# Kernel tuning notes

Hardware: AMD Instinct MI355X
Metric: run time of the kernel (lower is better)

Reference implementation:

```python
import jax, jax.numpy as jnp
import numpy as np

N_EMBD = 1024
N_HEADS = 16
HEAD_SIZE = N_EMBD // N_HEADS
BLOCK_SIZE = 2048
BATCH = 2
SEQ = 2048
EPS = 1e-5


def setup_inputs() -> dict:
    key = jax.random.key(0)
    ks = jax.random.split(key, 12)
    s = 0.02
    x = jax.random.normal(ks[0], (BATCH, SEQ, N_EMBD), dtype=jnp.float32)
    # per-head Q/K/V weights concatenated: [n_embd, n_heads*head_size]
    Wq = jax.random.normal(ks[1], (N_EMBD, N_EMBD), dtype=jnp.float32) * s
    Wk = jax.random.normal(ks[2], (N_EMBD, N_EMBD), dtype=jnp.float32) * s
    Wv = jax.random.normal(ks[3], (N_EMBD, N_EMBD), dtype=jnp.float32) * s
    Wproj = jax.random.normal(ks[4], (N_EMBD, N_EMBD), dtype=jnp.float32) * s
    bproj = jnp.zeros((N_EMBD,), dtype=jnp.float32)
    W1 = jax.random.normal(ks[5], (N_EMBD, 4 * N_EMBD), dtype=jnp.float32) * s
    b1 = jnp.zeros((4 * N_EMBD,), dtype=jnp.float32)
    W2 = jax.random.normal(ks[6], (4 * N_EMBD, N_EMBD), dtype=jnp.float32) * s
    b2 = jnp.zeros((N_EMBD,), dtype=jnp.float32)
    ln1_w = jnp.ones((N_EMBD,), dtype=jnp.float32)
    ln1_b = jnp.zeros((N_EMBD,), dtype=jnp.float32)
    ln2_w = jnp.ones((N_EMBD,), dtype=jnp.float32)
    ln2_b = jnp.zeros((N_EMBD,), dtype=jnp.float32)
    return dict(x=x, Wq=Wq, Wk=Wk, Wv=Wv, Wproj=Wproj, bproj=bproj,
                W1=W1, b1=b1, W2=W2, b2=b2,
                ln1_w=ln1_w, ln1_b=ln1_b, ln2_w=ln2_w, ln2_b=ln2_b)


def _layer_norm(x, w, b):
    mu = jnp.mean(x, axis=-1, keepdims=True)
    var = jnp.var(x, axis=-1, keepdims=True)
    return (x - mu) * jax.lax.rsqrt(var + EPS) * w + b


def reference(x, Wq, Wk, Wv, Wproj, bproj, W1, b1, W2, b2, ln1_w, ln1_b, ln2_w, ln2_b):
    B, T, C = x.shape
    # --- attention sub-block (pre-LN) ---
    h = _layer_norm(x, ln1_w, ln1_b)
    # project then split heads: [B,T,H,D] -> [B,H,T,D]
    def split(W):
        return (h @ W).reshape(B, T, N_HEADS, HEAD_SIZE).transpose(0, 2, 1, 3)
    q, k, v = split(Wq), split(Wk), split(Wv)
    # NOTE: original code scales by C**-0.5 with C = n_embd (not head_size)
    scores = jnp.einsum('bhtd,bhsd->bhts', q, k) * (C ** -0.5)  # [B,H,T,T]
    causal = jnp.tril(jnp.ones((T, T), dtype=bool))
    scores = jnp.where(causal, scores, -jnp.inf)
    wei = jax.nn.softmax(scores, axis=-1)
    attn = jnp.einsum('bhts,bhsd->bhtd', wei, v)  # [B,H,T,D]
    attn = attn.transpose(0, 2, 1, 3).reshape(B, T, C)  # concat heads
    x = x + attn @ Wproj + bproj
    # --- FFN sub-block (pre-LN) ---
    h2 = _layer_norm(x, ln2_w, ln2_b)
    ff = jax.nn.relu(h2 @ W1 + b1) @ W2 + b2
    return x + ff
```

## Files before the change

### kernel.cpp

```cpp
#include <hip/hip_runtime.h>
#include <cstdint>

typedef __attribute__((ext_vector_type(8))) __bf16 bf16_8;
typedef __attribute__((ext_vector_type(4))) __bf16 bf16_4;
typedef __attribute__((ext_vector_type(4))) float f32x4;

#define QSCALE 0.045084220027780106f

__device__ __forceinline__ void gld_lds16(const __bf16* g, __bf16* l) {
  __builtin_amdgcn_global_load_lds(
      (const __attribute__((address_space(1))) void*)(void*)g,
      (__attribute__((address_space(3))) void*)l, 16, 0, 0);
}

__global__ __launch_bounds__(256) void convt_k(
    const float* __restrict__ Wq, const float* __restrict__ Wk,
    const float* __restrict__ Wv, const float* __restrict__ Wp,
    const float* __restrict__ W1, const float* __restrict__ W2,
    __bf16* __restrict__ WqT, __bf16* __restrict__ WkT,
    __bf16* __restrict__ WvT, __bf16* __restrict__ WpT,
    __bf16* __restrict__ W1T, __bf16* __restrict__ W2T) {
  int bid = blockIdx.x;
  const float* in; __bf16* outp; int Kd, Nd, tile;
  if (bid < 4096) {
    int m = bid >> 10; tile = bid & 1023; Kd = 1024; Nd = 1024;
    in   = m == 0 ? Wq  : m == 1 ? Wk  : m == 2 ? Wv  : Wp;
    outp = m == 0 ? WqT : m == 1 ? WkT : m == 2 ? WvT : WpT;
  } else if (bid < 8192) {
    tile = bid - 4096; Kd = 1024; Nd = 4096; in = W1; outp = W1T;
  } else {
    tile = bid - 8192; Kd = 4096; Nd = 1024; in = W2; outp = W2T;
  }
  int tilesN = Nd >> 5;
  int tk = tile / tilesN, tn = tile % tilesN;
  int k0 = tk * 32, n0 = tn * 32;
  __shared__ float tbuf[32][33];
  int tx = threadIdx.x & 31, ty = threadIdx.x >> 5;
#pragma unroll
  for (int i = 0; i < 4; ++i)
    tbuf[ty + i * 8][tx] = in[(size_t)(k0 + ty + i * 8) * Nd + (n0 + tx)];
  __syncthreads();
#pragma unroll
  for (int i = 0; i < 4; ++i)
    outp[(size_t)(n0 + ty + i * 8) * Kd + (k0 + tx)] = (__bf16)tbuf[tx][ty + i * 8];
}

__global__ __launch_bounds__(256) void ln_k(const float* __restrict__ x,
                                            const float* __restrict__ w,
                                            const float* __restrict__ b,
                                            __bf16* __restrict__ out) {
  int row = blockIdx.x;
  int tid = threadIdx.x;
  f32x4 v = *(const f32x4*)(x + (size_t)row * 1024 + tid * 4);
  float s = v[0] + v[1] + v[2] + v[3];
  float sq = v[0] * v[0] + v[1] * v[1] + v[2] * v[2] + v[3] * v[3];
#pragma unroll
  for (int m = 1; m < 64; m <<= 1) { s += __shfl_xor(s, m); sq += __shfl_xor(sq, m); }
  __shared__ float rs[4], rq[4];
  int wave = tid >> 6, lane = tid & 63;
  if (lane == 0) { rs[wave] = s; rq[wave] = sq; }
  __syncthreads();
  s  = rs[0] + rs[1] + rs[2] + rs[3];
  sq = rq[0] + rq[1] + rq[2] + rq[3];
  float mu   = s * (1.f / 1024.f);
  float var  = sq * (1.f / 1024.f) - mu * mu;
  float rstd = rsqrtf(var + 1e-5f);
  f32x4 wv = *(const f32x4*)(w + tid * 4);
  f32x4 bv = *(const f32x4*)(b + tid * 4);
  bf16_4 o;
#pragma unroll
  for (int i = 0; i < 4; ++i) o[i] = (__bf16)((v[i] - mu) * rstd * wv[i] + bv[i]);
  *(bf16_4*)(out + (size_t)row * 1024 + tid * 4) = o;
}

template <int MODE, int BM, int BN, int BK>
__global__ __launch_bounds__(256) void gemm_k(
    const __bf16* __restrict__ A,
    const __bf16* __restrict__ B0, const __bf16* __restrict__ B1,
    const __bf16* __restrict__ B2,
    __bf16* __restrict__ O0, __bf16* __restrict__ O1, __bf16* __restrict__ O2,
    float* __restrict__ Of,
    const float* __restrict__ bias, const float* __restrict__ res,
    int K, int Nchunk, int nBlkM, int nBlkN) {
  constexpr int NC = BK / 8;
  constexpr int MT = BM / 32, NT = BN / 32;
  constexpr int KK = BK / 32;
  constexpr int RPC = 64 / NC;
  constexpr int CA = BM / RPC / 4;
  constexpr int CB = BN / RPC / 4;
  __shared__ __align__(16) __bf16 As[2][BM * BK];
  __shared__ __align__(16) __bf16 Bs[2][BN * BK];
  int chunk = blockIdx.y;
  const __bf16* Bt = chunk == 0 ? B0 : (chunk == 1 ? B1 : B2);
  __bf16* Ob       = chunk == 0 ? O0 : (chunk == 1 ? O1 : O2);
  int pid = blockIdx.x;
  const int GM = 8;
  int perG = GM * nBlkN;
  int gid = pid / perG;
  int fm = gid * GM;
  int gsz = min(nBlkM - fm, GM);
  int bm = fm + (pid % gsz);
  int bn = (pid % perG) / gsz;
  int m0 = bm * BM, n0 = bn * BN;
  int tid = threadIdx.x, wave = tid >> 6, lane = tid & 63;
  int quad = lane >> 4, l16 = lane & 15;
  int wm = (wave & 1) * (BM / 2), wn = (wave >> 1) * (BN / 2);
  int srow = lane / NC, schunk = lane % NC;

  f32x4 z = {0.f, 0.f, 0.f, 0.f};
  f32x4 acc[MT][NT];
#pragma unroll
  for (int mt = 0; mt < MT; ++mt)
#pragma unroll
    for (int nt = 0; nt < NT; ++nt) acc[mt][nt] = z;

  const __bf16* Ag = A  + (size_t)m0 * K;
  const __bf16* Bg = Bt + (size_t)n0 * K;

  auto stage = [&](int k0, int buf) {
#pragma unroll
    for (int i = 0; i < CA; ++i) {
      int r0 = (wave * CA + i) * RPC;
      int gc = schunk ^ ((r0 + srow) & (NC - 1));
      gld_lds16(Ag + (size_t)(r0 + srow) * K + k0 + gc * 8, &As[buf][r0 * BK]);
    }
#pragma unroll
    for (int i = 0; i < CB; ++i) {
      int r0 = (wave * CB + i) * RPC;
      int gc = schunk ^ ((r0 + srow) & (NC - 1));
      gld_lds16(Bg + (size_t)(r0 + srow) * K + k0 + gc * 8, &Bs[buf][r0 * BK]);
    }
  };

  auto compute = [&](int buf) {
#pragma unroll
    for (int kk = 0; kk < KK; ++kk) {
      bf16_8 af[MT], bfr[NT];
#pragma unroll
      for (int t = 0; t < MT; ++t) {
        int r = wm + t * 16 + l16;
        int lc = (kk * 4 + quad) ^ (r & (NC - 1));
        af[t] = *(const bf16_8*)(&As[buf][r * BK + lc * 8]);
      }
#pragma unroll
      for (int t = 0; t < NT; ++t) {
        int r = wn + t * 16 + l16;
        int lc = (kk * 4 + quad) ^ (r & (NC - 1));
        bfr[t] = *(const bf16_8*)(&Bs[buf][r * BK + lc * 8]);
      }
#pragma unroll
      for (int mt = 0; mt < MT; ++mt)
#pragma unroll
        for (int nt = 0; nt < NT; ++nt)
          acc[mt][nt] = __builtin_amdgcn_mfma_f32_16x16x32_bf16(af[mt], bfr[nt],
                                                                acc[mt][nt], 0, 0, 0);
    }
  };

  int niter = K / BK;
  stage(0, 0);
  __syncthreads();
  for (int it = 0; it < niter - 1; ++it) {
    stage((it + 1) * BK, (it + 1) & 1);
    compute(it & 1);
    __syncthreads();
  }
  compute((niter - 1) & 1);

  if (MODE == 0 && chunk == 2) {
#pragma unroll
    for (int mt = 0; mt < MT; ++mt) {
      int mbase = m0 + wm + mt * 16 + quad * 4;
      int bb = mbase >> 11, tt = mbase & 2047;
#pragma unroll
      for (int nt = 0; nt < NT; ++nt) {
        int n = n0 + wn + nt * 16 + l16;
        bf16_4 pk;
#pragma unroll
        for (int r = 0; r < 4; ++r) pk[r] = (__bf16)acc[mt][nt][r];
        *(bf16_4*)(O2 + ((size_t)((bb * 16 + (n >> 6)) * 64 + (n & 63))) * 2048 + tt) = pk;
      }
    }
    return;
  }

  float oscale = (MODE == 0 && chunk == 0) ? QSCALE : 1.0f;
#pragma unroll
  for (int mt = 0; mt < MT; ++mt) {
#pragma unroll
    for (int r = 0; r < 4; ++r) {
      int m = m0 + wm + mt * 16 + quad * 4 + r;
      size_t rowo = (size_t)m * Nchunk;
#pragma unroll
      for (int nt = 0; nt < NT; ++nt) {
        int n = n0 + wn + nt * 16 + l16;
        float v = acc[mt][nt][r];
        if (MODE == 0) {
          Ob[rowo + n] = (__bf16)(v * oscale);
        } else if (MODE == 1) {
          v += bias[n]; v = v > 0.f ? v : 0.f;
          Ob[rowo + n] = (__bf16)v;
        } else {
          v += bias[n] + res[rowo + n];
          Of[rowo + n] = v;
        }
      }
    }
  }
}

__global__ __launch_bounds__(256) void attn_k(const __bf16* __restrict__ Q,
                                              const __bf16* __restrict__ K,
                                              const __bf16* __restrict__ Vt,
                                              __bf16* __restrict__ O) {
  __shared__ __align__(16) __bf16 Kls[2][64 * 64];
  __shared__ __align__(16) __bf16 Vls[2][64 * 64];
  __shared__ __align__(16) __bf16 Pls[4][16 * 72];

  int blk = blockIdx.x;
  int qt = blk & 31, bh = blk >> 5;
  int h = bh & 15, b = bh >> 4;
  int q0 = qt * 64;
  int tid = threadIdx.x, wave = tid >> 6, lane = tid & 63;
  int quad = lane >> 4, l16 = lane & 15;
  int qw = q0 + wave * 16;
  int qrow = qw + l16;
  int r8 = lane >> 3, c8 = lane & 7;
  int cswz = c8 ^ r8;
  int so0 = (quad ^ (l16 & 7)) * 8;
  int so1 = so0 ^ 32;

  const __bf16* Qg = Q + ((size_t)(b * 2048 + qw + l16)) * 1024 + h * 64;
  bf16_8 qf0 = *(const bf16_8*)(Qg + quad * 8);
  bf16_8 qf1 = *(const bf16_8*)(Qg + 32 + quad * 8);

  const __bf16* Kb = K + (size_t)(b * 2048) * 1024 + h * 64;
  const __bf16* Vh = Vt + (size_t)((b * 16 + h) * 64) * 2048;

  f32x4 z = {0.f, 0.f, 0.f, 0.f};
  f32x4 ot[4];
#pragma unroll
  for (int dt = 0; dt < 4; ++dt) ot[dt] = z;
  float l_acc = 0.f;
  __bf16* Pw = &Pls[wave][0];

  auto stage = [&](int kt, int buf) {
#pragma unroll
    for (int i = 0; i < 2; ++i) {
      int rl = wave * 16 + i * 8 + r8;
      gld_lds16(Kb + (size_t)(kt + rl) * 1024 + cswz * 8,
                &Kls[buf][(wave * 16 + i * 8) * 64]);
      gld_lds16(Vh + (size_t)rl * 2048 + kt + cswz * 8,
                &Vls[buf][(wave * 16 + i * 8) * 64]);
    }
  };

  auto body = [&](int kt, int buf, bool masked) {
    f32x4 sf[4];
#pragma unroll
    for (int kk = 0; kk < 4; ++kk) {
      const __bf16* kr = &Kls[buf][(kk * 16 + l16) * 64];
      bf16_8 ka = *(const bf16_8*)(kr + so0);
      bf16_8 kb = *(const bf16_8*)(kr + so1);
      f32x4 a = z;
      a = __builtin_amdgcn_mfma_f32_16x16x32_bf16(ka, qf0, a, 0, 0, 0);
      a = __builtin_amdgcn_mfma_f32_16x16x32_bf16(kb, qf1, a, 0, 0, 0);
      sf[kk] = a;
    }
#pragma unroll
    for (int kk = 0; kk < 4; ++kk) {
      bf16_4 pk;
#pragma unroll
      for (int r = 0; r < 4; ++r) {
        float x = sf[kk][r];
        if (masked && (kt + kk * 16 + quad * 4 + r > qrow)) x = -1e30f;
        float p = __builtin_amdgcn_exp2f(x);
        l_acc += p;
        pk[r] = (__bf16)p;
      }
      *(bf16_4*)(Pw + l16 * 72 + kk * 16 + quad * 4) = pk;
    }
    bf16_8 pf0 = *(const bf16_8*)(Pw + l16 * 72 + quad * 8);
    bf16_8 pf1 = *(const bf16_8*)(Pw + l16 * 72 + 32 + quad * 8);
#pragma unroll
    for (int dt = 0; dt < 4; ++dt) {
      const __bf16* vr = &Vls[buf][(dt * 16 + l16) * 64];
      bf16_8 v0 = *(const bf16_8*)(vr + so0);
      bf16_8 v1 = *(const bf16_8*)(vr + so1);
      ot[dt] = __builtin_amdgcn_mfma_f32_16x16x32_bf16(v0, pf0, ot[dt], 0, 0, 0);
      ot[dt] = __builtin_amdgcn_mfma_f32_16x16x32_bf16(v1, pf1, ot[dt], 0, 0, 0);
    }
  };

  stage(0, 0);
  __syncthreads();
  int cur = 0;
  for (int it = 0; it < qt; ++it) {
    stage((it + 1) * 64, cur ^ 1);
    body(it * 64, cur, false);
    __syncthreads();
    cur ^= 1;
  }
  body(qt * 64, cur, true);

  float l = l_acc;
  l += __shfl_xor(l, 16);
  l += __shfl_xor(l, 32);
  float inv = 1.0f / l;
  size_t base = (size_t)(b * 2048 + qw + l16) * 1024 + h * 64;
#pragma unroll
  for (int dt = 0; dt < 4; ++dt) {
    bf16_4 ok;
#pragma unroll
    for (int r = 0; r < 4; ++r) ok[r] = (__bf16)(ot[dt][r] * inv);
    *(bf16_4*)(O + base + dt * 16 + quad * 4) = ok;
  }
}

extern "C" void kernel_launch(void* const* d_in, const int* in_sizes, int n_in,
                              void* d_out, int out_size, void* d_ws,
                              size_t ws_size, hipStream_t stream) {
  const float* x   = (const float*)d_in[0];
  const float* Wq  = (const float*)d_in[1];
  const float* Wk  = (const float*)d_in[2];
  const float* Wv  = (const float*)d_in[3];
  const float* Wp  = (const float*)d_in[4];
  const float* bp  = (const float*)d_in[5];
  const float* W1  = (const float*)d_in[6];
  const float* b1  = (const float*)d_in[7];
  const float* W2  = (const float*)d_in[8];
  const float* b2  = (const float*)d_in[9];
  const float* l1w = (const float*)d_in[10];
  const float* l1b = (const float*)d_in[11];
  const float* l2w = (const float*)d_in[12];
  const float* l2b = (const float*)d_in[13];
  float* out = (float*)d_out;
  char* ws = (char*)d_ws;
  const size_t MB = 1024ull * 1024ull;
  __bf16* WqT = (__bf16*)(ws + 0 * MB);
  __bf16* WkT = (__bf16*)(ws + 2 * MB);
  __bf16* WvT = (__bf16*)(ws + 4 * MB);
  __bf16* WpT = (__bf16*)(ws + 6 * MB);
  __bf16* W1T = (__bf16*)(ws + 8 * MB);
  __bf16* W2T = (__bf16*)(ws + 16 * MB);
  __bf16* hb  = (__bf16*)(ws + 24 * MB);
  __bf16* Qb  = (__bf16*)(ws + 32 * MB);
  __bf16* Kb_ = (__bf16*)(ws + 40 * MB);
  __bf16* Vt  = (__bf16*)(ws + 48 * MB);
  __bf16* Ab  = (__bf16*)(ws + 56 * MB);
  __bf16* F1  = (__bf16*)(ws + 64 * MB);

  convt_k<<<12288, 256, 0, stream>>>(Wq, Wk, Wv, Wp, W1, W2,
                                     WqT, WkT, WvT, WpT, W1T, W2T);
  ln_k<<<4096, 256, 0, stream>>>(x, l1w, l1b, hb);
  gemm_k<0, 128, 128, 32><<<dim3(256, 3), 256, 0, stream>>>(
      hb, WqT, WkT, WvT, Qb, Kb_, Vt, nullptr, nullptr, nullptr,
      1024, 1024, 32, 8);
  attn_k<<<1024, 256, 0, stream>>>(Qb, Kb_, Vt, Ab);
  gemm_k<2, 64, 64, 64><<<dim3(1024, 1), 256, 0, stream>>>(
      Ab, WpT, WpT, WpT, nullptr, nullptr, nullptr, out, bp, x,
      1024, 1024, 64, 16);
  ln_k<<<4096, 256, 0, stream>>>(out, l2w, l2b, hb);
  gemm_k<1, 128, 128, 32><<<dim3(1024, 1), 256, 0, stream>>>(
      hb, W1T, W1T, W1T, F1, F1, F1, nullptr, b1, nullptr,
      1024, 4096, 32, 32);
  gemm_k<2, 64, 64, 64><<<dim3(1024, 1), 256, 0, stream>>>(
      F1, W2T, W2T, W2T, nullptr, nullptr, nullptr, out, b2, out,
      4096, 1024, 64, 16);
}
```

Measured before the change: 356.8 us.

## Enlarge attention query tile to 128 rows and schedule heavy causal tiles first

```diff
diff --git a/kernel.cpp b/kernel.cpp
--- a/kernel.cpp
+++ b/kernel.cpp
@@ -215,105 +215,128 @@
                                               __bf16* __restrict__ O) {
   __shared__ __align__(16) __bf16 Kls[2][64 * 64];
   __shared__ __align__(16) __bf16 Vls[2][64 * 64];
-  __shared__ __align__(16) __bf16 Pls[4][16 * 72];
-
-  int blk = blockIdx.x;
-  int qt = blk & 31, bh = blk >> 5;
+  __shared__ __align__(16) __bf16 Pls[4][32 * 72];
+
+  int i = blockIdx.x;
+  int qt, bh;
+  if (i < 256) { qt = 15 - (i >> 5); bh = i & 31; }
+  else         { qt = (i - 256) >> 5; bh = i & 31; }
   int h = bh & 15, b = bh >> 4;
-  int q0 = qt * 64;
+  int q0 = qt * 128;
   int tid = threadIdx.x, wave = tid >> 6, lane = tid & 63;
   int quad = lane >> 4, l16 = lane & 15;
-  int qw = q0 + wave * 16;
-  int qrow = qw + l16;
+  int qw = q0 + wave * 32;
   int r8 = lane >> 3, c8 = lane & 7;
   int cswz = c8 ^ r8;
   int so0 = (quad ^ (l16 & 7)) * 8;
   int so1 = so0 ^ 32;
 
-  const __bf16* Qg = Q + ((size_t)(b * 2048 + qw + l16)) * 1024 + h * 64;
-  bf16_8 qf0 = *(const bf16_8*)(Qg + quad * 8);
-  bf16_8 qf1 = *(const bf16_8*)(Qg + 32 + quad * 8);
+  bf16_8 qf[2][2];
+#pragma unroll
+  for (int g = 0; g < 2; ++g) {
+    const __bf16* Qg = Q + ((size_t)(b * 2048 + qw + g * 16 + l16)) * 1024 + h * 64;
+    qf[g][0] = *(const bf16_8*)(Qg + quad * 8);
+    qf[g][1] = *(const bf16_8*)(Qg + 32 + quad * 8);
+  }
 
   const __bf16* Kb = K + (size_t)(b * 2048) * 1024 + h * 64;
   const __bf16* Vh = Vt + (size_t)((b * 16 + h) * 64) * 2048;
 
   f32x4 z = {0.f, 0.f, 0.f, 0.f};
-  f32x4 ot[4];
-#pragma unroll
-  for (int dt = 0; dt < 4; ++dt) ot[dt] = z;
-  float l_acc = 0.f;
+  f32x4 ot[2][4];
+#pragma unroll
+  for (int g = 0; g < 2; ++g)
+#pragma unroll
+    for (int dt = 0; dt < 4; ++dt) ot[g][dt] = z;
+  float l_acc[2] = {0.f, 0.f};
   __bf16* Pw = &Pls[wave][0];
 
   auto stage = [&](int kt, int buf) {
 #pragma unroll
-    for (int i = 0; i < 2; ++i) {
-      int rl = wave * 16 + i * 8 + r8;
+    for (int i2 = 0; i2 < 2; ++i2) {
+      int rl = wave * 16 + i2 * 8 + r8;
       gld_lds16(Kb + (size_t)(kt + rl) * 1024 + cswz * 8,
-                &Kls[buf][(wave * 16 + i * 8) * 64]);
+                &Kls[buf][(wave * 16 + i2 * 8) * 64]);
       gld_lds16(Vh + (size_t)rl * 2048 + kt + cswz * 8,
-                &Vls[buf][(wave * 16 + i * 8) * 64]);
+                &Vls[buf][(wave * 16 + i2 * 8) * 64]);
     }
   };
 
-  auto body = [&](int kt, int buf, bool masked) {
-    f32x4 sf[4];
-#pragma unroll
-    for (int kk = 0; kk < 4; ++kk) {
-      const __bf16* kr = &Kls[buf][(kk * 16 + l16) * 64];
-      bf16_8 ka = *(const bf16_8*)(kr + so0);
-      bf16_8 kb = *(const bf16_8*)(kr + so1);
-      f32x4 a = z;
-      a = __builtin_amdgcn_mfma_f32_16x16x32_bf16(ka, qf0, a, 0, 0, 0);
-      a = __builtin_amdgcn_mfma_f32_16x16x32_bf16(kb, qf1, a, 0, 0, 0);
-      sf[kk] = a;
-    }
-#pragma unroll
-    for (int kk = 0; kk < 4; ++kk) {
-      bf16_4 pk;
-#pragma unroll
-      for (int r = 0; r < 4; ++r) {
-        float x = sf[kk][r];
-        if (masked && (kt + kk * 16 + quad * 4 + r > qrow)) x = -1e30f;
-        float p = __builtin_amdgcn_exp2f(x);
-        l_acc += p;
-        pk[r] = (__bf16)p;
-      }
-      *(bf16_4*)(Pw + l16 * 72 + kk * 16 + quad * 4) = pk;
-    }
-    bf16_8 pf0 = *(const bf16_8*)(Pw + l16 * 72 + quad * 8);
-    bf16_8 pf1 = *(const bf16_8*)(Pw + l16 * 72 + 32 + quad * 8);
-#pragma unroll
-    for (int dt = 0; dt < 4; ++dt) {
-      const __bf16* vr = &Vls[buf][(dt * 16 + l16) * 64];
-      bf16_8 v0 = *(const bf16_8*)(vr + so0);
-      bf16_8 v1 = *(const bf16_8*)(vr + so1);
-      ot[dt] = __builtin_amdgcn_mfma_f32_16x16x32_bf16(v0, pf0, ot[dt], 0, 0, 0);
-      ot[dt] = __builtin_amdgcn_mfma_f32_16x16x32_bf16(v1, pf1, ot[dt], 0, 0, 0);
-    }
-  };
-
+  int ntiles = 2 * (qt + 1);
   stage(0, 0);
   __syncthreads();
-  int cur = 0;
-  for (int it = 0; it < qt; ++it) {
-    stage((it + 1) * 64, cur ^ 1);
-    body(it * 64, cur, false);
+  for (int it = 0; it < ntiles; ++it) {
+    int kt = it * 64;
+    int buf = it & 1;
+    if (it + 1 < ntiles) stage((it + 1) * 64, buf ^ 1);
+    if (kt <= qw + 31) {
+      bool masked = (kt + 63 > qw);
+      f32x4 sf[2][4];
+#pragma unroll
+      for (int kk = 0; kk < 4; ++kk) {
+        const __bf16* kr = &Kls[buf][(kk * 16 + l16) * 64];
+        bf16_8 ka = *(const bf16_8*)(kr + so0);
+        bf16_8 kb = *(const bf16_8*)(kr + so1);
+#pragma unroll
+        for (int g = 0; g < 2; ++g) {
+          f32x4 a = z;
+          a = __builtin_amdgcn_mfma_f32_16x16x32_bf16(ka, qf[g][0], a, 0, 0, 0);
+          a = __builtin_amdgcn_mfma_f32_16x16x32_bf16(kb, qf[g][1], a, 0, 0, 0);
+          sf[g][kk] = a;
+        }
+      }
+#pragma unroll
+      for (int g = 0; g < 2; ++g) {
+        int qrow = qw + g * 16 + l16;
+#pragma unroll
+        for (int kk = 0; kk < 4; ++kk) {
+          bf16_4 pk;
+#pragma unroll
+          for (int r = 0; r < 4; ++r) {
+            float x = sf[g][kk][r];
+            if (masked && (kt + kk * 16 + quad * 4 + r > qrow)) x = -1e30f;
+            float p = __builtin_amdgcn_exp2f(x);
+            l_acc[g] += p;
+            pk[r] = (__bf16)p;
+          }
+          *(bf16_4*)(Pw + (g * 16 + l16) * 72 + kk * 16 + quad * 4) = pk;
+        }
+      }
+      bf16_8 pf[2][2];
+#pragma unroll
+      for (int g = 0; g < 2; ++g) {
+        pf[g][0] = *(const bf16_8*)(Pw + (g * 16 + l16) * 72 + quad * 8);
+        pf[g][1] = *(const bf16_8*)(Pw + (g * 16 + l16) * 72 + 32 + quad * 8);
+      }
+#pragma unroll
+      for (int dt = 0; dt < 4; ++dt) {
+        const __bf16* vr = &Vls[buf][(dt * 16 + l16) * 64];
+        bf16_8 v0 = *(const bf16_8*)(vr + so0);
+        bf16_8 v1 = *(const bf16_8*)(vr + so1);
+#pragma unroll
+        for (int g = 0; g < 2; ++g) {
+          ot[g][dt] = __builtin_amdgcn_mfma_f32_16x16x32_bf16(v0, pf[g][0], ot[g][dt], 0, 0, 0);
+          ot[g][dt] = __builtin_amdgcn_mfma_f32_16x16x32_bf16(v1, pf[g][1], ot[g][dt], 0, 0, 0);
+        }
+      }
+    }
     __syncthreads();
-    cur ^= 1;
-  }
-  body(qt * 64, cur, true);
-
-  float l = l_acc;
-  l += __shfl_xor(l, 16);
-  l += __shfl_xor(l, 32);
-  float inv = 1.0f / l;
-  size_t base = (size_t)(b * 2048 + qw + l16) * 1024 + h * 64;
-#pragma unroll
-  for (int dt = 0; dt < 4; ++dt) {
-    bf16_4 ok;
-#pragma unroll
-    for (int r = 0; r < 4; ++r) ok[r] = (__bf16)(ot[dt][r] * inv);
-    *(bf16_4*)(O + base + dt * 16 + quad * 4) = ok;
+  }
+
+#pragma unroll
+  for (int g = 0; g < 2; ++g) {
+    float l = l_acc[g];
+    l += __shfl_xor(l, 16);
+    l += __shfl_xor(l, 32);
+    float inv = 1.0f / l;
+    size_t base = (size_t)(b * 2048 + qw + g * 16 + l16) * 1024 + h * 64;
+#pragma unroll
+    for (int dt = 0; dt < 4; ++dt) {
+      bf16_4 ok;
+#pragma unroll
+      for (int r = 0; r < 4; ++r) ok[r] = (__bf16)(ot[g][dt][r] * inv);
+      *(bf16_4*)(O + base + dt * 16 + quad * 4) = ok;
+    }
   }
 }
 
@@ -356,7 +379,7 @@
   gemm_k<0, 128, 128, 32><<<dim3(256, 3), 256, 0, stream>>>(
       hb, WqT, WkT, WvT, Qb, Kb_, Vt, nullptr, nullptr, nullptr,
       1024, 1024, 32, 8);
-  attn_k<<<1024, 256, 0, stream>>>(Qb, Kb_, Vt, Ab);
+  attn_k<<<512, 256, 0, stream>>>(Qb, Kb_, Vt, Ab);
   gemm_k<2, 64, 64, 64><<<dim3(1024, 1), 256, 0, stream>>>(
       Ab, WpT, WpT, WpT, nullptr, nullptr, nullptr, out, bp, x,
       1024, 1024, 64, 16);
```

After: 341.9 us. 4.2% less time.
